# Kernel optimization log

Hardware: AMD Instinct MI355X
Metric: run time of the kernel (lower is better)

The kernel has to match this reference:

```python
import jax, jax.numpy as jnp
import numpy as np

N_NODES = 50000
N_EDGES = 800000
D_IN, D_HID, D_OUT = 128, 128, 64
BN_EPS = 1e-5


def gcn_conv(x, W, b, src, dst, ew, n):
    # PyG GCNConv: out[i] = sum_j norm_ij * (x @ W)[j] + b, with self-loops added
    xw = x @ W                                   # [N, D_out]
    loop = jnp.arange(n)
    s = jnp.concatenate([src, loop])             # add self-loops (weight 1)
    d = jnp.concatenate([dst, loop])
    w = jnp.concatenate([ew, jnp.ones((n,), x.dtype)])
    deg = jax.ops.segment_sum(w, d, num_segments=n)
    dinv = jnp.where(deg > 0, jax.lax.rsqrt(deg), 0.0)
    norm = dinv[s] * w * dinv[d]                 # symmetric normalization
    msg = xw[s] * norm[:, None]                  # gather + scale  [E+N, D_out]
    return jax.ops.segment_sum(msg, d, num_segments=n) + b


def setup_inputs() -> dict:
    key = jax.random.key(0)
    ks = jax.random.split(key, 12)
    x = jax.random.normal(ks[0], (N_NODES, D_IN), dtype=jnp.float32)
    edge_index = jax.random.randint(ks[1], (2, N_EDGES), 0, N_NODES, dtype=jnp.int64)
    edge_weight = jax.random.uniform(ks[2], (N_EDGES,), dtype=jnp.float32)
    W1 = jax.random.normal(ks[3], (D_IN, D_HID), dtype=jnp.float32) * 0.05
    b1 = jnp.zeros((D_HID,), jnp.float32)
    gamma = jnp.ones((D_HID,), jnp.float32)
    beta = jnp.zeros((D_HID,), jnp.float32)
    running_mean = jax.random.normal(ks[4], (D_HID,), dtype=jnp.float32) * 0.1
    running_var = jax.random.uniform(ks[5], (D_HID,), dtype=jnp.float32) + 0.5
    W2 = jax.random.normal(ks[6], (D_HID, D_OUT), dtype=jnp.float32) * 0.05
    b2 = jnp.zeros((D_OUT,), jnp.float32)
    return {"x": x, "edge_index": edge_index, "edge_weight": edge_weight,
            "W1": W1, "b1": b1, "gamma": gamma, "beta": beta,
            "running_mean": running_mean, "running_var": running_var,
            "W2": W2, "b2": b2}


def reference(x, edge_index, edge_weight, W1, b1, gamma, beta,
              running_mean, running_var, W2, b2):
    src, dst = edge_index[0], edge_index[1]
    n = x.shape[0]
    h = gcn_conv(x, W1, b1, src, dst, edge_weight, n)
    # BatchNorm1d in eval mode (running stats); dropout inactive in eval
    h = (h - running_mean) * jax.lax.rsqrt(running_var + BN_EPS) * gamma + beta
    h = jax.nn.relu(h)
    out = gcn_conv(h, W2, b2, src, dst, edge_weight, n)
    return out
```

## Files before the change

### kernel.cpp

```cpp
#include <hip/hip_runtime.h>
#include <hip/hip_fp16.h>

#define BN_EPS 1e-5f
#define PAD 64
#define CAP 4608

typedef __attribute__((ext_vector_type(8))) short short8;
typedef __attribute__((ext_vector_type(4))) float f32x4;

static __device__ __forceinline__ unsigned short f2bf(float f) {
    unsigned u = __float_as_uint(f);
    u += 0x7FFF + ((u >> 16) & 1);
    return (unsigned short)(u >> 16);
}
static __device__ __forceinline__ float bf2f(unsigned short b) {
    return __uint_as_float((unsigned)b << 16);
}
static __device__ __forceinline__ unsigned pk(int s, float w) {
    return ((unsigned)s << 16) | (unsigned)__half_as_ushort(__float2half_rn(w));
}
static __device__ __forceinline__ float pw(unsigned e) {
    return __half2float(__ushort_as_half((unsigned short)(e & 0xFFFFu)));
}

__global__ __launch_bounds__(256) void k_fused(const int* __restrict__ src, const int* __restrict__ dst,
                                               const float* __restrict__ ew,
                                               uint2* __restrict__ bins, int* __restrict__ gcnt,
                                               int e, int gfill, int stride, int nb,
                                               const float* __restrict__ A, const float* __restrict__ W,
                                               unsigned short* __restrict__ C, int n,
                                               const float* __restrict__ b1, const float* __restrict__ gamma,
                                               const float* __restrict__ beta, const float* __restrict__ mean,
                                               const float* __restrict__ var,
                                               float* __restrict__ bnscale, float* __restrict__ bnshift,
                                               const float* __restrict__ W2, unsigned short* __restrict__ w2bf) {
    __shared__ unsigned short W1s[16384];
    int tid = threadIdx.x;
    int b = (int)blockIdx.x;
    int gGemm = (n + 63) / 64;

    bool isFill = ((b % stride) == 0) && (b / stride < gfill);
    if (isFill) {
        int*   lcnt   = (int*)W1s;
        int*   gbase  = lcnt + 256;
        int*   loff   = gbase + 256;
        uint2* sorted = (uint2*)(loff + 256);
        lcnt[tid] = 0;
        __syncthreads();

        int i0 = ((b / stride) * 256 + tid) * 8;
        unsigned pv[8];  int bk[8]; int rk[8]; unsigned dl[8];
        int cnt8 = 0;
        if (i0 + 7 < e) {
            int4   s0 = *(const int4*)(src + i0), s1 = *(const int4*)(src + i0 + 4);
            int4   d0 = *(const int4*)(dst + i0), d1 = *(const int4*)(dst + i0 + 4);
            float4 w0 = *(const float4*)(ew + i0), w1 = *(const float4*)(ew + i0 + 4);
            int   ss[8] = {s0.x, s0.y, s0.z, s0.w, s1.x, s1.y, s1.z, s1.w};
            int   dd[8] = {d0.x, d0.y, d0.z, d0.w, d1.x, d1.y, d1.z, d1.w};
            float ww[8] = {w0.x, w0.y, w0.z, w0.w, w1.x, w1.y, w1.z, w1.w};
            #pragma unroll
            for (int j = 0; j < 8; ++j) {
                int d_ = dd[j];
                bk[j] = d_ >> 8;
                dl[j] = (unsigned)(d_ & 255);
                rk[j] = atomicAdd(&lcnt[bk[j]], 1);
                pv[j] = pk(ss[j], ww[j]);
            }
            cnt8 = 8;
        } else {
            for (int j = 0; j < 8; ++j) {
                int i = i0 + j;
                if (i < e) {
                    int d_ = dst[i];
                    bk[j] = d_ >> 8;
                    dl[j] = (unsigned)(d_ & 255);
                    rk[j] = atomicAdd(&lcnt[bk[j]], 1);
                    pv[j] = pk(src[i], ew[i]);
                    cnt8 = j + 1;
                }
            }
        }
        __syncthreads();
        if (tid < nb) gbase[tid] = atomicAdd(&gcnt[tid], lcnt[tid]);
        int li = lcnt[tid];
        loff[tid] = li;
        __syncthreads();
        #pragma unroll
        for (int off = 1; off < 256; off <<= 1) {
            int v = (tid >= off) ? loff[tid - off] : 0;
            __syncthreads();
            loff[tid] += v;
            __syncthreads();
        }
        int excl = loff[tid] - li;
        __syncthreads();
        loff[tid] = excl;
        __syncthreads();
        for (int j = 0; j < cnt8; ++j) {
            int pos  = gbase[bk[j]] + rk[j];
            int sidx = loff[bk[j]] + rk[j];
            unsigned gp = (pos < CAP) ? ((unsigned)(bk[j] * CAP + pos) | (dl[j] << 24))
                                      : 0xFFFFFFFFu;
            sorted[sidx] = make_uint2(pv[j], gp);
        }
        __syncthreads();
        int total = loff[255] + lcnt[255];
        for (int i = tid; i < total; i += 256) {
            uint2 s = sorted[i];
            if (s.y != 0xFFFFFFFFu)
                bins[s.y & 0x00FFFFFFu] = make_uint2(s.x, s.y >> 24);
        }
        return;
    }

    int fillsBefore = (b == 0) ? 0 : min(gfill, (b - 1) / stride + 1);
    int g = b - fillsBefore;
    if (g == gGemm) {
        if (tid < 128) {
            float sc = gamma[tid] * rsqrtf(var[tid] + BN_EPS);
            bnscale[tid] = sc;
            bnshift[tid] = (b1[tid] - mean[tid]) * sc + beta[tid];
        }
        #pragma unroll
        for (int q = 0; q < 4; ++q) {
            int s = tid * 4 + q;
            int kk = s >> 8, nt = (s >> 6) & 3, lane = s & 63;
            int kb = kk * 32 + ((lane >> 4) << 3);
            int nc = (nt << 4) + (lane & 15);
            ushort4 o0, o1;
            o0.x = f2bf(W2[(kb + 0) * 64 + nc]);
            o0.y = f2bf(W2[(kb + 1) * 64 + nc]);
            o0.z = f2bf(W2[(kb + 2) * 64 + nc]);
            o0.w = f2bf(W2[(kb + 3) * 64 + nc]);
            o1.x = f2bf(W2[(kb + 4) * 64 + nc]);
            o1.y = f2bf(W2[(kb + 5) * 64 + nc]);
            o1.z = f2bf(W2[(kb + 6) * 64 + nc]);
            o1.w = f2bf(W2[(kb + 7) * 64 + nc]);
            ((ushort4*)w2bf)[s * 2]     = o0;
            ((ushort4*)w2bf)[s * 2 + 1] = o1;
        }
        return;
    }

    int row0 = g * 64;

    {
        int k  = tid >> 1;
        int c0 = (tid & 1) * 64;
        int kk = k >> 5, lg = (k >> 3) & 3, ii = k & 7;
        int tbase = kk * 4096 + lg * 128 + ii;
        const float4* Wr = (const float4*)(W + (size_t)k * 128 + c0);
        #pragma unroll
        for (int j = 0; j < 16; ++j) {
            float4 v = Wr[j];
            int n0 = c0 + j * 4;
            W1s[tbase + ((n0 + 0) >> 4) * 512 + ((n0 + 0) & 15) * 8] = f2bf(v.x);
            W1s[tbase + ((n0 + 1) >> 4) * 512 + ((n0 + 1) & 15) * 8] = f2bf(v.y);
            W1s[tbase + ((n0 + 2) >> 4) * 512 + ((n0 + 2) & 15) * 8] = f2bf(v.z);
            W1s[tbase + ((n0 + 3) >> 4) * 512 + ((n0 + 3) & 15) * 8] = f2bf(v.w);
        }
    }
    __syncthreads();

    int w = tid >> 6, lane = tid & 63;
    int arow = row0 + w * 16 + (lane & 15);
    if (arow > n - 1) arow = n - 1;
    const float* xrow = A + (size_t)arow * 128 + ((lane >> 4) * 8);
    const unsigned short* Wl = W1s + (size_t)lane * 8;

    f32x4 z = {0.f, 0.f, 0.f, 0.f};
    f32x4 acc0 = z, acc1 = z, acc2 = z, acc3 = z, acc4 = z, acc5 = z, acc6 = z, acc7 = z;

    #pragma unroll
    for (int kk = 0; kk < 4; ++kk) {
        float4 v0 = *(const float4*)(xrow + kk * 32);
        float4 v1 = *(const float4*)(xrow + kk * 32 + 4);
        short8 a;
        a[0] = (short)f2bf(v0.x); a[1] = (short)f2bf(v0.y);
        a[2] = (short)f2bf(v0.z); a[3] = (short)f2bf(v0.w);
        a[4] = (short)f2bf(v1.x); a[5] = (short)f2bf(v1.y);
        a[6] = (short)f2bf(v1.z); a[7] = (short)f2bf(v1.w);
        const unsigned short* Wk = Wl + kk * 4096;
        short8 b0 = *(const short8*)(Wk);
        short8 b1 = *(const short8*)(Wk + 512);
        short8 b2 = *(const short8*)(Wk + 1024);
        short8 b3 = *(const short8*)(Wk + 1536);
        short8 b4 = *(const short8*)(Wk + 2048);
        short8 b5 = *(const short8*)(Wk + 2560);
        short8 b6 = *(const short8*)(Wk + 3072);
        short8 b7 = *(const short8*)(Wk + 3584);
        acc0 = __builtin_amdgcn_mfma_f32_16x16x32_bf16(a, b0, acc0, 0, 0, 0);
        acc1 = __builtin_amdgcn_mfma_f32_16x16x32_bf16(a, b1, acc1, 0, 0, 0);
        acc2 = __builtin_amdgcn_mfma_f32_16x16x32_bf16(a, b2, acc2, 0, 0, 0);
        acc3 = __builtin_amdgcn_mfma_f32_16x16x32_bf16(a, b3, acc3, 0, 0, 0);
        acc4 = __builtin_amdgcn_mfma_f32_16x16x32_bf16(a, b4, acc4, 0, 0, 0);
        acc5 = __builtin_amdgcn_mfma_f32_16x16x32_bf16(a, b5, acc5, 0, 0, 0);
        acc6 = __builtin_amdgcn_mfma_f32_16x16x32_bf16(a, b6, acc6, 0, 0, 0);
        acc7 = __builtin_amdgcn_mfma_f32_16x16x32_bf16(a, b7, acc7, 0, 0, 0);
    }

    int rw = row0 + w * 16 + ((lane >> 4) << 2);
    int cb = lane & 15;
    #define STORE_NT(av, nt)                                                              \
        if (rw + 0 < n) C[(size_t)(rw + 0) * 128 + (nt)*16 + cb] = f2bf(av[0]);           \
        if (rw + 1 < n) C[(size_t)(rw + 1) * 128 + (nt)*16 + cb] = f2bf(av[1]);           \
        if (rw + 2 < n) C[(size_t)(rw + 2) * 128 + (nt)*16 + cb] = f2bf(av[2]);           \
        if (rw + 3 < n) C[(size_t)(rw + 3) * 128 + (nt)*16 + cb] = f2bf(av[3]);
    STORE_NT(acc0, 0) STORE_NT(acc1, 1) STORE_NT(acc2, 2) STORE_NT(acc3, 3)
    STORE_NT(acc4, 4) STORE_NT(acc5, 5) STORE_NT(acc6, 6) STORE_NT(acc7, 7)
    #undef STORE_NT
}

__global__ __launch_bounds__(256) void k_csr(const uint2* __restrict__ bins, const int* __restrict__ gcnt,
                                             unsigned* __restrict__ pad, int* __restrict__ cnt,
                                             float* __restrict__ dinv, int n) {
    __shared__ unsigned csr[256 * PAD];
    __shared__ int lc[256];
    int tid = threadIdx.x;
    int b = (int)blockIdx.x;
    int node0 = b << 8;
    int nodes = min(256, n - node0);
    lc[tid] = 0;
    __syncthreads();

    int m = gcnt[b];
    if (m > CAP) m = CAP;
    const uint2* seg = bins + (size_t)b * CAP;
    for (int i = tid; i < m; i += 256) {
        uint2 v = seg[i];
        int r = atomicAdd(&lc[v.y], 1);
        if (r < PAD) csr[v.y * PAD + r] = v.x;
    }
    __syncthreads();

    if (tid < nodes) {
        int c = lc[tid];
        cnt[node0 + tid] = c;
        int cc = min(c, PAD);
        float s = 1.0f;
        for (int p = 0; p < cc; ++p) s += pw(csr[tid * PAD + p]);
        dinv[node0 + tid] = rsqrtf(s);
    }
    const uint4* s4 = (const uint4*)csr;
    uint4* d4 = (uint4*)(pad + (size_t)node0 * PAD);
    int tot = nodes * (PAD / 4);
    for (int q = tid; q < tot; q += 256) d4[q] = s4[q];
}

__global__ __launch_bounds__(256) void k_scale(unsigned* __restrict__ pad, const int* __restrict__ cnt,
                                               const float* __restrict__ dinv, int n) {
    int gid = blockIdx.x * 256 + threadIdx.x;
    int node = gid >> 2, q = gid & 3;
    if (node >= n) return;
    int c = min(cnt[node], PAD);
    int p0 = q * 16, p1 = min(p0 + 16, c);
    size_t base = (size_t)node * PAD;
    for (int p = p0; p < p1; ++p) {
        unsigned e = pad[base + p];
        float w = pw(e) * dinv[e >> 16];
        pad[base + p] = (e & 0xFFFF0000u) | (unsigned)__half_as_ushort(__float2half_rn(w));
    }
}

__global__ __launch_bounds__(256) void k_h(const unsigned short* __restrict__ xw, const int* __restrict__ cnt,
                                           const unsigned* __restrict__ pad,
                                           const float* __restrict__ dinv,
                                           const float* __restrict__ scale, const float* __restrict__ shift,
                                           unsigned* __restrict__ h, int n) {
    int grp = threadIdx.x >> 5;
    int lc  = threadIdx.x & 31;
    int node = blockIdx.x * 8 + grp;
    if (node >= n) return;
    const ushort4* X4 = (const ushort4*)xw;
    float di = dinv[node];
    int c = min(cnt[node], PAD);
    size_t base = (size_t)node * PAD;
    ushort4 q0 = X4[(size_t)node * 32 + lc];
    float4 acc0 = make_float4(bf2f(q0.x) * di, bf2f(q0.y) * di, bf2f(q0.z) * di, bf2f(q0.w) * di);
    float4 acc1 = make_float4(0, 0, 0, 0);
    float4 acc2 = make_float4(0, 0, 0, 0);
    float4 acc3 = make_float4(0, 0, 0, 0);
    int p = 0;
    for (; p + 7 < c; p += 8) {
        uint4 ea = *(const uint4*)(pad + base + p);
        uint4 eb = *(const uint4*)(pad + base + p + 4);
        ushort4 r0 = X4[(size_t)(ea.x >> 16) * 32 + lc];
        ushort4 r1 = X4[(size_t)(ea.y >> 16) * 32 + lc];
        ushort4 r2 = X4[(size_t)(ea.z >> 16) * 32 + lc];
        ushort4 r3 = X4[(size_t)(ea.w >> 16) * 32 + lc];
        ushort4 r4 = X4[(size_t)(eb.x >> 16) * 32 + lc];
        ushort4 r5 = X4[(size_t)(eb.y >> 16) * 32 + lc];
        ushort4 r6 = X4[(size_t)(eb.z >> 16) * 32 + lc];
        ushort4 r7 = X4[(size_t)(eb.w >> 16) * 32 + lc];
        float w0 = pw(ea.x), w1 = pw(ea.y), w2 = pw(ea.z), w3 = pw(ea.w);
        float w4 = pw(eb.x), w5 = pw(eb.y), w6 = pw(eb.z), w7 = pw(eb.w);
        acc0.x += w0 * bf2f(r0.x); acc0.y += w0 * bf2f(r0.y); acc0.z += w0 * bf2f(r0.z); acc0.w += w0 * bf2f(r0.w);
        acc1.x += w1 * bf2f(r1.x); acc1.y += w1 * bf2f(r1.y); acc1.z += w1 * bf2f(r1.z); acc1.w += w1 * bf2f(r1.w);
        acc2.x += w2 * bf2f(r2.x); acc2.y += w2 * bf2f(r2.y); acc2.z += w2 * bf2f(r2.z); acc2.w += w2 * bf2f(r2.w);
        acc3.x += w3 * bf2f(r3.x); acc3.y += w3 * bf2f(r3.y); acc3.z += w3 * bf2f(r3.z); acc3.w += w3 * bf2f(r3.w);
        acc0.x += w4 * bf2f(r4.x); acc0.y += w4 * bf2f(r4.y); acc0.z += w4 * bf2f(r4.z); acc0.w += w4 * bf2f(r4.w);
        acc1.x += w5 * bf2f(r5.x); acc1.y += w5 * bf2f(r5.y); acc1.z += w5 * bf2f(r5.z); acc1.w += w5 * bf2f(r5.w);
        acc2.x += w6 * bf2f(r6.x); acc2.y += w6 * bf2f(r6.y); acc2.z += w6 * bf2f(r6.z); acc2.w += w6 * bf2f(r6.w);
        acc3.x += w7 * bf2f(r7.x); acc3.y += w7 * bf2f(r7.y); acc3.z += w7 * bf2f(r7.z); acc3.w += w7 * bf2f(r7.w);
    }
    for (; p + 3 < c; p += 4) {
        uint4 ea = *(const uint4*)(pad + base + p);
        ushort4 r0 = X4[(size_t)(ea.x >> 16) * 32 + lc];
        ushort4 r1 = X4[(size_t)(ea.y >> 16) * 32 + lc];
        ushort4 r2 = X4[(size_t)(ea.z >> 16) * 32 + lc];
        ushort4 r3 = X4[(size_t)(ea.w >> 16) * 32 + lc];
        float w0 = pw(ea.x), w1 = pw(ea.y), w2 = pw(ea.z), w3 = pw(ea.w);
        acc0.x += w0 * bf2f(r0.x); acc0.y += w0 * bf2f(r0.y); acc0.z += w0 * bf2f(r0.z); acc0.w += w0 * bf2f(r0.w);
        acc1.x += w1 * bf2f(r1.x); acc1.y += w1 * bf2f(r1.y); acc1.z += w1 * bf2f(r1.z); acc1.w += w1 * bf2f(r1.w);
        acc2.x += w2 * bf2f(r2.x); acc2.y += w2 * bf2f(r2.y); acc2.z += w2 * bf2f(r2.z); acc2.w += w2 * bf2f(r2.w);
        acc3.x += w3 * bf2f(r3.x); acc3.y += w3 * bf2f(r3.y); acc3.z += w3 * bf2f(r3.z); acc3.w += w3 * bf2f(r3.w);
    }
    for (; p < c; ++p) {
        unsigned e0 = pad[base + p];
        float w0 = pw(e0);
        ushort4 a = X4[(size_t)(e0 >> 16) * 32 + lc];
        acc0.x += w0 * bf2f(a.x); acc0.y += w0 * bf2f(a.y); acc0.z += w0 * bf2f(a.z); acc0.w += w0 * bf2f(a.w);
    }
    acc0.x = (acc0.x + acc1.x + acc2.x + acc3.x) * di;
    acc0.y = (acc0.y + acc1.y + acc2.y + acc3.y) * di;
    acc0.z = (acc0.z + acc1.z + acc2.z + acc3.z) * di;
    acc0.w = (acc0.w + acc1.w + acc2.w + acc3.w) * di;
    float4 Sc = ((const float4*)scale)[lc];
    float4 Sh = ((const float4*)shift)[lc];
    unsigned short r0 = f2bf(fmaxf(acc0.x * Sc.x + Sh.x, 0.0f));
    unsigned short r1 = f2bf(fmaxf(acc0.y * Sc.y + Sh.y, 0.0f));
    unsigned short r2 = f2bf(fmaxf(acc0.z * Sc.z + Sh.z, 0.0f));
    unsigned short r3 = f2bf(fmaxf(acc0.w * Sc.w + Sh.w, 0.0f));
    unsigned hu0 = ((unsigned)r1 << 16) | (unsigned)r0;
    unsigned hu1 = ((unsigned)r3 << 16) | (unsigned)r2;
    *(uint2*)(h + (size_t)node * 64 + lc * 2) = make_uint2(hu0, hu1);
}

__global__ __launch_bounds__(256) void k_gemm2(const unsigned short* __restrict__ h,
                                               const unsigned short* __restrict__ w2bf,
                                               unsigned short* __restrict__ hw2, int n) {
    __shared__ unsigned short W2f[8192];
    int tid = threadIdx.x;
    {
        const uint4* s4 = (const uint4*)w2bf;
        uint4* d4 = (uint4*)W2f;
        #pragma unroll
        for (int q = 0; q < 4; ++q) d4[q * 256 + tid] = s4[q * 256 + tid];
    }
    __syncthreads();

    int w = tid >> 6, lane = tid & 63;
    int row0 = (int)blockIdx.x * 64 + w * 16;
    int ar = row0 + (lane & 15);
    if (ar > n - 1) ar = n - 1;
    const unsigned short* hr = h + (size_t)ar * 128 + ((lane >> 4) * 8);
    const unsigned short* Wl = W2f + (size_t)lane * 8;

    f32x4 z = {0.f, 0.f, 0.f, 0.f};
    f32x4 acc0 = z, acc1 = z, acc2 = z, acc3 = z;
    #pragma unroll
    for (int kk = 0; kk < 4; ++kk) {
        short8 a = *(const short8*)(hr + kk * 32);
        const unsigned short* Wk = Wl + kk * 2048;
        short8 b0 = *(const short8*)(Wk);
        short8 b1 = *(const short8*)(Wk + 512);
        short8 b2 = *(const short8*)(Wk + 1024);
        short8 b3 = *(const short8*)(Wk + 1536);
        acc0 = __builtin_amdgcn_mfma_f32_16x16x32_bf16(a, b0, acc0, 0, 0, 0);
        acc1 = __builtin_amdgcn_mfma_f32_16x16x32_bf16(a, b1, acc1, 0, 0, 0);
        acc2 = __builtin_amdgcn_mfma_f32_16x16x32_bf16(a, b2, acc2, 0, 0, 0);
        acc3 = __builtin_amdgcn_mfma_f32_16x16x32_bf16(a, b3, acc3, 0, 0, 0);
    }
    int rw = row0 + ((lane >> 4) << 2);
    int cb = lane & 15;
    #define ST_NT(av, nt)                                                                 \
        if (rw + 0 < n) hw2[(size_t)(rw + 0) * 64 + (nt)*16 + cb] = f2bf(av[0]);          \
        if (rw + 1 < n) hw2[(size_t)(rw + 1) * 64 + (nt)*16 + cb] = f2bf(av[1]);          \
        if (rw + 2 < n) hw2[(size_t)(rw + 2) * 64 + (nt)*16 + cb] = f2bf(av[2]);          \
        if (rw + 3 < n) hw2[(size_t)(rw + 3) * 64 + (nt)*16 + cb] = f2bf(av[3]);
    ST_NT(acc0, 0) ST_NT(acc1, 1) ST_NT(acc2, 2) ST_NT(acc3, 3)
    #undef ST_NT
}

__global__ __launch_bounds__(256) void k_agg2(const unsigned short* __restrict__ hw, const int* __restrict__ cnt,
                                              const unsigned* __restrict__ pad,
                                              const float* __restrict__ dinv,
                                              const float* __restrict__ b2, float* __restrict__ out, int n) {
    int node = blockIdx.x * 16 + (threadIdx.x >> 4);
    if (node >= n) return;
    int lc = threadIdx.x & 15;
    const ushort4* X4 = (const ushort4*)hw;
    float di = dinv[node];
    int c = min(cnt[node], PAD);
    size_t base = (size_t)node * PAD;
    ushort4 q0 = X4[(size_t)node * 16 + lc];
    float4 acc0 = make_float4(bf2f(q0.x) * di, bf2f(q0.y) * di, bf2f(q0.z) * di, bf2f(q0.w) * di);
    float4 acc1 = make_float4(0, 0, 0, 0);
    float4 acc2 = make_float4(0, 0, 0, 0);
    float4 acc3 = make_float4(0, 0, 0, 0);
    int p = 0;
    for (; p + 7 < c; p += 8) {
        uint4 ea = *(const uint4*)(pad + base + p);
        uint4 eb = *(const uint4*)(pad + base + p + 4);
        ushort4 r0 = X4[(size_t)(ea.x >> 16) * 16 + lc];
        ushort4 r1 = X4[(size_t)(ea.y >> 16) * 16 + lc];
        ushort4 r2 = X4[(size_t)(ea.z >> 16) * 16 + lc];
        ushort4 r3 = X4[(size_t)(ea.w >> 16) * 16 + lc];
        ushort4 r4 = X4[(size_t)(eb.x >> 16) * 16 + lc];
        ushort4 r5 = X4[(size_t)(eb.y >> 16) * 16 + lc];
        ushort4 r6 = X4[(size_t)(eb.z >> 16) * 16 + lc];
        ushort4 r7 = X4[(size_t)(eb.w >> 16) * 16 + lc];
        float w0 = pw(ea.x), w1 = pw(ea.y), w2 = pw(ea.z), w3 = pw(ea.w);
        float w4 = pw(eb.x), w5 = pw(eb.y), w6 = pw(eb.z), w7 = pw(eb.w);
        acc0.x += w0 * bf2f(r0.x); acc0.y += w0 * bf2f(r0.y); acc0.z += w0 * bf2f(r0.z); acc0.w += w0 * bf2f(r0.w);
        acc1.x += w1 * bf2f(r1.x); acc1.y += w1 * bf2f(r1.y); acc1.z += w1 * bf2f(r1.z); acc1.w += w1 * bf2f(r1.w);
        acc2.x += w2 * bf2f(r2.x); acc2.y += w2 * bf2f(r2.y); acc2.z += w2 * bf2f(r2.z); acc2.w += w2 * bf2f(r2.w);
        acc3.x += w3 * bf2f(r3.x); acc3.y += w3 * bf2f(r3.y); acc3.z += w3 * bf2f(r3.z); acc3.w += w3 * bf2f(r3.w);
        acc0.x += w4 * bf2f(r4.x); acc0.y += w4 * bf2f(r4.y); acc0.z += w4 * bf2f(r4.z); acc0.w += w4 * bf2f(r4.w);
        acc1.x += w5 * bf2f(r5.x); acc1.y += w5 * bf2f(r5.y); acc1.z += w5 * bf2f(r5.z); acc1.w += w5 * bf2f(r5.w);
        acc2.x += w6 * bf2f(r6.x); acc2.y += w6 * bf2f(r6.y); acc2.z += w6 * bf2f(r6.z); acc2.w += w6 * bf2f(r6.w);
        acc3.x += w7 * bf2f(r7.x); acc3.y += w7 * bf2f(r7.y); acc3.z += w7 * bf2f(r7.z); acc3.w += w7 * bf2f(r7.w);
    }
    for (; p + 3 < c; p += 4) {
        uint4 ea = *(const uint4*)(pad + base + p);
        ushort4 r0 = X4[(size_t)(ea.x >> 16) * 16 + lc];
        ushort4 r1 = X4[(size_t)(ea.y >> 16) * 16 + lc];
        ushort4 r2 = X4[(size_t)(ea.z >> 16) * 16 + lc];
        ushort4 r3 = X4[(size_t)(ea.w >> 16) * 16 + lc];
        float w0 = pw(ea.x), w1 = pw(ea.y), w2 = pw(ea.z), w3 = pw(ea.w);
        acc0.x += w0 * bf2f(r0.x); acc0.y += w0 * bf2f(r0.y); acc0.z += w0 * bf2f(r0.z); acc0.w += w0 * bf2f(r0.w);
        acc1.x += w1 * bf2f(r1.x); acc1.y += w1 * bf2f(r1.y); acc1.z += w1 * bf2f(r1.z); acc1.w += w1 * bf2f(r1.w);
        acc2.x += w2 * bf2f(r2.x); acc2.y += w2 * bf2f(r2.y); acc2.z += w2 * bf2f(r2.z); acc2.w += w2 * bf2f(r2.w);
        acc3.x += w3 * bf2f(r3.x); acc3.y += w3 * bf2f(r3.y); acc3.z += w3 * bf2f(r3.z); acc3.w += w3 * bf2f(r3.w);
    }
    for (; p < c; ++p) {
        unsigned e0 = pad[base + p];
        float w0 = pw(e0);
        ushort4 a = X4[(size_t)(e0 >> 16) * 16 + lc];
        acc0.x += w0 * bf2f(a.x); acc0.y += w0 * bf2f(a.y); acc0.z += w0 * bf2f(a.z); acc0.w += w0 * bf2f(a.w);
    }
    float4 B = ((const float4*)b2)[lc];
    acc0.x = (acc0.x + acc1.x + acc2.x + acc3.x) * di + B.x;
    acc0.y = (acc0.y + acc1.y + acc2.y + acc3.y) * di + B.y;
    acc0.z = (acc0.z + acc1.z + acc2.z + acc3.z) * di + B.z;
    acc0.w = (acc0.w + acc1.w + acc2.w + acc3.w) * di + B.w;
    ((float4*)out)[(size_t)node * 16 + lc] = acc0;
}


extern "C" void kernel_launch(void* const* d_in, const int* in_sizes, int n_in,
                              void* d_out, int out_size, void* d_ws, size_t ws_size,
                              hipStream_t stream) {
    const float* x     = (const float*)d_in[0];
    const int*   ei    = (const int*)d_in[1];
    const float* ew    = (const float*)d_in[2];
    const float* W1    = (const float*)d_in[3];
    const float* b1    = (const float*)d_in[4];
    const float* gamma = (const float*)d_in[5];
    const float* beta  = (const float*)d_in[6];
    const float* rmean = (const float*)d_in[7];
    const float* rvar  = (const float*)d_in[8];
    const float* W2    = (const float*)d_in[9];
    const float* b2    = (const float*)d_in[10];
    float* out = (float*)d_out;

    int N = in_sizes[0] / 128;
    int E = in_sizes[2];
    const int* src = ei;
    const int* dst = ei + E;
    int NB = (N + 255) >> 8;

    char* p = (char*)d_ws;
    auto carve = [&](size_t bytes) { char* q = p; p += (bytes + 255) & ~(size_t)255; return (void*)q; };
    int*      cnt     = (int*)     carve(sizeof(int) * (size_t)N);
    unsigned* pad     = (unsigned*)carve(sizeof(unsigned) * (size_t)N * PAD);
    float*    dinv    = (float*)   carve(sizeof(float) * (size_t)N);
    float*    bnscale = (float*)   carve(sizeof(float) * 128);
    float*    bnshift = (float*)   carve(sizeof(float) * 128);
    unsigned short* w2bf = (unsigned short*)carve(sizeof(unsigned short) * 128 * 64);
    unsigned short* xw1  = (unsigned short*)carve(sizeof(unsigned short) * (size_t)N * 128);
    unsigned*       hbuf = (unsigned*)      carve(sizeof(unsigned) * (size_t)N * 64);
    unsigned short* hw2  = (unsigned short*)carve(sizeof(unsigned short) * (size_t)N * 64);
    int*      gcnt    = (int*)     carve(sizeof(int) * (size_t)NB);
    uint2*    bins    = (uint2*)   carve(sizeof(uint2) * (size_t)NB * CAP);

    int gFill = (E + 2047) / 2048;
    int gGemm = (N + 63) / 64;
    int T     = gFill + gGemm + 1;
    int S     = T / gFill;
    if (S < 2) S = 2;

    hipMemsetAsync(gcnt, 0, sizeof(int) * (size_t)NB, stream);
    k_fused <<<T, 256, 0, stream>>>(src, dst, ew, bins, gcnt, E, gFill, S, NB,
                                    x, W1, xw1, N,
                                    b1, gamma, beta, rmean, rvar, bnscale, bnshift,
                                    W2, w2bf);
    k_csr   <<<NB, 256, 0, stream>>>(bins, gcnt, pad, cnt, dinv, N);
    k_scale <<<(N * 4 + 255) / 256, 256, 0, stream>>>(pad, cnt, dinv, N);
    k_h     <<<(N + 7) / 8, 256, 0, stream>>>(xw1, cnt, pad, dinv, bnscale, bnshift, hbuf, N);
    k_gemm2 <<<(N + 63) / 64, 256, 0, stream>>>((const unsigned short*)hbuf, w2bf, hw2, N);
    k_agg2  <<<(N + 15) / 16, 256, 0, stream>>>(hw2, cnt, pad, dinv, b2, out, N);
}
```

Measured before the change: 188.8 us.

## Split GEMM1 columns across blocks, halve fill work, widen aggregation gathers

The fused kernel now splits the first GEMM into two 64-column halves per row tile, which halves the shared weight tile and doubles the number of GEMM blocks. Each fill block now bins 4 edges per thread instead of 8, again doubling the block count. Both aggregation kernels now use 16-byte gathers with 8 bf16 features per lane, so each node uses fewer lanes and each block covers more nodes. The 8-wide unrolled edge loop is dropped in favour of a 4-wide loop. The aim is more parallelism and fewer, wider memory transactions, at the cost of more bin atomics and less memory-level parallelism per thread.

```diff
diff --git a/kernel.cpp b/kernel.cpp
--- a/kernel.cpp
+++ b/kernel.cpp
@@ -22,6 +22,15 @@
 static __device__ __forceinline__ float pw(unsigned e) {
     return __half2float(__ushort_as_half((unsigned short)(e & 0xFFFFu)));
 }
+static __device__ __forceinline__ void upk8(uint4 v, float4& a, float4& b) {
+    a.x = bf2f((unsigned short)(v.x & 0xFFFFu)); a.y = bf2f((unsigned short)(v.x >> 16));
+    a.z = bf2f((unsigned short)(v.y & 0xFFFFu)); a.w = bf2f((unsigned short)(v.y >> 16));
+    b.x = bf2f((unsigned short)(v.z & 0xFFFFu)); b.y = bf2f((unsigned short)(v.z >> 16));
+    b.z = bf2f((unsigned short)(v.w & 0xFFFFu)); b.w = bf2f((unsigned short)(v.w >> 16));
+}
+#define FMA8(wv, ra, rb, A, B)                                            \
+    A.x += (wv) * ra.x; A.y += (wv) * ra.y; A.z += (wv) * ra.z; A.w += (wv) * ra.w; \
+    B.x += (wv) * rb.x; B.y += (wv) * rb.y; B.z += (wv) * rb.z; B.w += (wv) * rb.w;
 
 __global__ __launch_bounds__(256) void k_fused(const int* __restrict__ src, const int* __restrict__ dst,
                                                const float* __restrict__ ew,
@@ -34,10 +43,10 @@
                                                const float* __restrict__ var,
                                                float* __restrict__ bnscale, float* __restrict__ bnshift,
                                                const float* __restrict__ W2, unsigned short* __restrict__ w2bf) {
-    __shared__ unsigned short W1s[16384];
+    __shared__ unsigned short W1s[8192];
     int tid = threadIdx.x;
     int b = (int)blockIdx.x;
-    int gGemm = (n + 63) / 64;
+    int gGemm = ((n + 63) / 64) * 2;
 
     bool isFill = ((b % stride) == 0) && (b / stride < gfill);
     if (isFill) {
@@ -48,27 +57,27 @@
         lcnt[tid] = 0;
         __syncthreads();
 
-        int i0 = ((b / stride) * 256 + tid) * 8;
-        unsigned pv[8];  int bk[8]; int rk[8]; unsigned dl[8];
-        int cnt8 = 0;
-        if (i0 + 7 < e) {
-            int4   s0 = *(const int4*)(src + i0), s1 = *(const int4*)(src + i0 + 4);
-            int4   d0 = *(const int4*)(dst + i0), d1 = *(const int4*)(dst + i0 + 4);
-            float4 w0 = *(const float4*)(ew + i0), w1 = *(const float4*)(ew + i0 + 4);
-            int   ss[8] = {s0.x, s0.y, s0.z, s0.w, s1.x, s1.y, s1.z, s1.w};
-            int   dd[8] = {d0.x, d0.y, d0.z, d0.w, d1.x, d1.y, d1.z, d1.w};
-            float ww[8] = {w0.x, w0.y, w0.z, w0.w, w1.x, w1.y, w1.z, w1.w};
+        int i0 = ((b / stride) * 256 + tid) * 4;
+        unsigned pv[4];  int bk[4]; int rk[4]; unsigned dl[4];
+        int cnt4 = 0;
+        if (i0 + 3 < e) {
+            int4   s0 = *(const int4*)(src + i0);
+            int4   d0 = *(const int4*)(dst + i0);
+            float4 w0 = *(const float4*)(ew + i0);
+            int   ss[4] = {s0.x, s0.y, s0.z, s0.w};
+            int   dd[4] = {d0.x, d0.y, d0.z, d0.w};
+            float ww[4] = {w0.x, w0.y, w0.z, w0.w};
             #pragma unroll
-            for (int j = 0; j < 8; ++j) {
+            for (int j = 0; j < 4; ++j) {
                 int d_ = dd[j];
                 bk[j] = d_ >> 8;
                 dl[j] = (unsigned)(d_ & 255);
                 rk[j] = atomicAdd(&lcnt[bk[j]], 1);
                 pv[j] = pk(ss[j], ww[j]);
             }
-            cnt8 = 8;
+            cnt4 = 4;
         } else {
-            for (int j = 0; j < 8; ++j) {
+            for (int j = 0; j < 4; ++j) {
                 int i = i0 + j;
                 if (i < e) {
                     int d_ = dst[i];
@@ -76,7 +85,7 @@
                     dl[j] = (unsigned)(d_ & 255);
                     rk[j] = atomicAdd(&lcnt[bk[j]], 1);
                     pv[j] = pk(src[i], ew[i]);
-                    cnt8 = j + 1;
+                    cnt4 = j + 1;
                 }
             }
         }
@@ -96,7 +105,7 @@
         __syncthreads();
         loff[tid] = excl;
         __syncthreads();
-        for (int j = 0; j < cnt8; ++j) {
+        for (int j = 0; j < cnt4; ++j) {
             int pos  = gbase[bk[j]] + rk[j];
             int sidx = loff[bk[j]] + rk[j];
             unsigned gp = (pos < CAP) ? ((unsigned)(bk[j] * CAP + pos) | (dl[j] << 24))
@@ -142,18 +151,19 @@
         return;
     }
 
-    int row0 = g * 64;
+    int rt = g >> 1, ch = g & 1;
+    int row0 = rt * 64, c0 = ch * 64;
 
     {
         int k  = tid >> 1;
-        int c0 = (tid & 1) * 64;
+        int h0 = (tid & 1) * 32;
         int kk = k >> 5, lg = (k >> 3) & 3, ii = k & 7;
-        int tbase = kk * 4096 + lg * 128 + ii;
-        const float4* Wr = (const float4*)(W + (size_t)k * 128 + c0);
+        int tbase = kk * 2048 + lg * 128 + ii;
+        const float4* Wr = (const float4*)(W + (size_t)k * 128 + c0 + h0);
         #pragma unroll
-        for (int j = 0; j < 16; ++j) {
+        for (int j = 0; j < 8; ++j) {
             float4 v = Wr[j];
-            int n0 = c0 + j * 4;
+            int n0 = h0 + j * 4;
             W1s[tbase + ((n0 + 0) >> 4) * 512 + ((n0 + 0) & 15) * 8] = f2bf(v.x);
             W1s[tbase + ((n0 + 1) >> 4) * 512 + ((n0 + 1) & 15) * 8] = f2bf(v.y);
             W1s[tbase + ((n0 + 2) >> 4) * 512 + ((n0 + 2) & 15) * 8] = f2bf(v.z);
@@ -169,7 +179,7 @@
     const unsigned short* Wl = W1s + (size_t)lane * 8;
 
     f32x4 z = {0.f, 0.f, 0.f, 0.f};
-    f32x4 acc0 = z, acc1 = z, acc2 = z, acc3 = z, acc4 = z, acc5 = z, acc6 = z, acc7 = z;
+    f32x4 acc0 = z, acc1 = z, acc2 = z, acc3 = z;
 
     #pragma unroll
     for (int kk = 0; kk < 4; ++kk) {
@@ -180,34 +190,25 @@
         a[2] = (short)f2bf(v0.z); a[3] = (short)f2bf(v0.w);
         a[4] = (short)f2bf(v1.x); a[5] = (short)f2bf(v1.y);
         a[6] = (short)f2bf(v1.z); a[7] = (short)f2bf(v1.w);
-        const unsigned short* Wk = Wl + kk * 4096;
+        const unsigned short* Wk = Wl + kk * 2048;
         short8 b0 = *(const short8*)(Wk);
         short8 b1 = *(const short8*)(Wk + 512);
         short8 b2 = *(const short8*)(Wk + 1024);
         short8 b3 = *(const short8*)(Wk + 1536);
-        short8 b4 = *(const short8*)(Wk + 2048);
-        short8 b5 = *(const short8*)(Wk + 2560);
-        short8 b6 = *(const short8*)(Wk + 3072);
-        short8 b7 = *(const short8*)(Wk + 3584);
         acc0 = __builtin_amdgcn_mfma_f32_16x16x32_bf16(a, b0, acc0, 0, 0, 0);
         acc1 = __builtin_amdgcn_mfma_f32_16x16x32_bf16(a, b1, acc1, 0, 0, 0);
         acc2 = __builtin_amdgcn_mfma_f32_16x16x32_bf16(a, b2, acc2, 0, 0, 0);
         acc3 = __builtin_amdgcn_mfma_f32_16x16x32_bf16(a, b3, acc3, 0, 0, 0);
-        acc4 = __builtin_amdgcn_mfma_f32_16x16x32_bf16(a, b4, acc4, 0, 0, 0);
-        acc5 = __builtin_amdgcn_mfma_f32_16x16x32_bf16(a, b5, acc5, 0, 0, 0);
-        acc6 = __builtin_amdgcn_mfma_f32_16x16x32_bf16(a, b6, acc6, 0, 0, 0);
-        acc7 = __builtin_amdgcn_mfma_f32_16x16x32_bf16(a, b7, acc7, 0, 0, 0);
     }
 
     int rw = row0 + w * 16 + ((lane >> 4) << 2);
-    int cb = lane & 15;
+    int cb = c0 + (lane & 15);
     #define STORE_NT(av, nt)                                                              \
         if (rw + 0 < n) C[(size_t)(rw + 0) * 128 + (nt)*16 + cb] = f2bf(av[0]);           \
         if (rw + 1 < n) C[(size_t)(rw + 1) * 128 + (nt)*16 + cb] = f2bf(av[1]);           \
         if (rw + 2 < n) C[(size_t)(rw + 2) * 128 + (nt)*16 + cb] = f2bf(av[2]);           \
         if (rw + 3 < n) C[(size_t)(rw + 3) * 128 + (nt)*16 + cb] = f2bf(av[3]);
     STORE_NT(acc0, 0) STORE_NT(acc1, 1) STORE_NT(acc2, 2) STORE_NT(acc3, 3)
-    STORE_NT(acc4, 4) STORE_NT(acc5, 5) STORE_NT(acc6, 6) STORE_NT(acc7, 7)
     #undef STORE_NT
 }
 
@@ -267,73 +268,67 @@
                                            const float* __restrict__ dinv,
                                            const float* __restrict__ scale, const float* __restrict__ shift,
                                            unsigned* __restrict__ h, int n) {
-    int grp = threadIdx.x >> 5;
-    int lc  = threadIdx.x & 31;
-    int node = blockIdx.x * 8 + grp;
+    int grp = threadIdx.x >> 4;
+    int lc  = threadIdx.x & 15;
+    int node = blockIdx.x * 16 + grp;
     if (node >= n) return;
-    const ushort4* X4 = (const ushort4*)xw;
+    const uint4* X = (const uint4*)xw;
     float di = dinv[node];
     int c = min(cnt[node], PAD);
     size_t base = (size_t)node * PAD;
-    ushort4 q0 = X4[(size_t)node * 32 + lc];
-    float4 acc0 = make_float4(bf2f(q0.x) * di, bf2f(q0.y) * di, bf2f(q0.z) * di, bf2f(q0.w) * di);
-    float4 acc1 = make_float4(0, 0, 0, 0);
-    float4 acc2 = make_float4(0, 0, 0, 0);
-    float4 acc3 = make_float4(0, 0, 0, 0);
+    float4 ra, rb;
+    upk8(X[(size_t)node * 16 + lc], ra, rb);
+    float4 A0 = make_float4(ra.x * di, ra.y * di, ra.z * di, ra.w * di);
+    float4 B0 = make_float4(rb.x * di, rb.y * di, rb.z * di, rb.w * di);
+    float4 A1 = make_float4(0, 0, 0, 0), B1 = A1;
+    float4 A2 = A1, B2 = A1, A3 = A1, B3 = A1;
     int p = 0;
-    for (; p + 7 < c; p += 8) {
-        uint4 ea = *(const uint4*)(pad + base + p);
-        uint4 eb = *(const uint4*)(pad + base + p + 4);
-        ushort4 r0 = X4[(size_t)(ea.x >> 16) * 32 + lc];
-        ushort4 r1 = X4[(size_t)(ea.y >> 16) * 32 + lc];
-        ushort4 r2 = X4[(size_t)(ea.z >> 16) * 32 + lc];
-        ushort4 r3 = X4[(size_t)(ea.w >> 16) * 32 + lc];
-        ushort4 r4 = X4[(size_t)(eb.x >> 16) * 32 + lc];
-        ushort4 r5 = X4[(size_t)(eb.y >> 16) * 32 + lc];
-        ushort4 r6 = X4[(size_t)(eb.z >> 16) * 32 + lc];
-        ushort4 r7 = X4[(size_t)(eb.w >> 16) * 32 + lc];
-        float w0 = pw(ea.x), w1 = pw(ea.y), w2 = pw(ea.z), w3 = pw(ea.w);
-        float w4 = pw(eb.x), w5 = pw(eb.y), w6 = pw(eb.z), w7 = pw(eb.w);
-        acc0.x += w0 * bf2f(r0.x); acc0.y += w0 * bf2f(r0.y); acc0.z += w0 * bf2f(r0.z); acc0.w += w0 * bf2f(r0.w);
-        acc1.x += w1 * bf2f(r1.x); acc1.y += w1 * bf2f(r1.y); acc1.z += w1 * bf2f(r1.z); acc1.w += w1 * bf2f(r1.w);
-        acc2.x += w2 * bf2f(r2.x); acc2.y += w2 * bf2f(r2.y); acc2.z += w2 * bf2f(r2.z); acc2.w += w2 * bf2f(r2.w);
-        acc3.x += w3 * bf2f(r3.x); acc3.y += w3 * bf2f(r3.y); acc3.z += w3 * bf2f(r3.z); acc3.w += w3 * bf2f(r3.w);
-        acc0.x += w4 * bf2f(r4.x); acc0.y += w4 * bf2f(r4.y); acc0.z += w4 * bf2f(r4.z); acc0.w += w4 * bf2f(r4.w);
-        acc1.x += w5 * bf2f(r5.x); acc1.y += w5 * bf2f(r5.y); acc1.z += w5 * bf2f(r5.z); acc1.w += w5 * bf2f(r5.w);
-        acc2.x += w6 * bf2f(r6.x); acc2.y += w6 * bf2f(r6.y); acc2.z += w6 * bf2f(r6.z); acc2.w += w6 * bf2f(r6.w);
-        acc3.x += w7 * bf2f(r7.x); acc3.y += w7 * bf2f(r7.y); acc3.z += w7 * bf2f(r7.z); acc3.w += w7 * bf2f(r7.w);
-    }
     for (; p + 3 < c; p += 4) {
-        uint4 ea = *(const uint4*)(pad + base + p);
-        ushort4 r0 = X4[(size_t)(ea.x >> 16) * 32 + lc];
-        ushort4 r1 = X4[(size_t)(ea.y >> 16) * 32 + lc];
-        ushort4 r2 = X4[(size_t)(ea.z >> 16) * 32 + lc];
-        ushort4 r3 = X4[(size_t)(ea.w >> 16) * 32 + lc];
-        float w0 = pw(ea.x), w1 = pw(ea.y), w2 = pw(ea.z), w3 = pw(ea.w);
-        acc0.x += w0 * bf2f(r0.x); acc0.y += w0 * bf2f(r0.y); acc0.z += w0 * bf2f(r0.z); acc0.w += w0 * bf2f(r0.w);
-        acc1.x += w1 * bf2f(r1.x); acc1.y += w1 * bf2f(r1.y); acc1.z += w1 * bf2f(r1.z); acc1.w += w1 * bf2f(r1.w);
-        acc2.x += w2 * bf2f(r2.x); acc2.y += w2 * bf2f(r2.y); acc2.z += w2 * bf2f(r2.z); acc2.w += w2 * bf2f(r2.w);
-        acc3.x += w3 * bf2f(r3.x); acc3.y += w3 * bf2f(r3.y); acc3.z += w3 * bf2f(r3.z); acc3.w += w3 * bf2f(r3.w);
+        uint4 ee = *(const uint4*)(pad + base + p);
+        uint4 r0 = X[(size_t)(ee.x >> 16) * 16 + lc];
+        uint4 r1 = X[(size_t)(ee.y >> 16) * 16 + lc];
+        uint4 r2 = X[(size_t)(ee.z >> 16) * 16 + lc];
+        uint4 r3 = X[(size_t)(ee.w >> 16) * 16 + lc];
+        float w0 = pw(ee.x), w1 = pw(ee.y), w2 = pw(ee.z), w3 = pw(ee.w);
+        float4 a, b;
+        upk8(r0, a, b); FMA8(w0, a, b, A0, B0);
+        upk8(r1, a, b); FMA8(w1, a, b, A1, B1);
+        upk8(r2, a, b); FMA8(w2, a, b, A2, B2);
+        upk8(r3, a, b); FMA8(w3, a, b, A3, B3);
     }
     for (; p < c; ++p) {
         unsigned e0 = pad[base + p];
         float w0 = pw(e0);
-        ushort4 a = X4[(size_t)(e0 >> 16) * 32 + lc];
-        acc0.x += w0 * bf2f(a.x); acc0.y += w0 * bf2f(a.y); acc0.z += w0 * bf2f(a.z); acc0.w += w0 * bf2f(a.w);
-    }
-    acc0.x = (acc0.x + acc1.x + acc2.x + acc3.x) * di;
-    acc0.y = (acc0.y + acc1.y + acc2.y + acc3.y) * di;
-    acc0.z = (acc0.z + acc1.z + acc2.z + acc3.z) * di;
-    acc0.w = (acc0.w + acc1.w + acc2.w + acc3.w) * di;
-    float4 Sc = ((const float4*)scale)[lc];
-    float4 Sh = ((const float4*)shift)[lc];
-    unsigned short r0 = f2bf(fmaxf(acc0.x * Sc.x + Sh.x, 0.0f));
-    unsigned short r1 = f2bf(fmaxf(acc0.y * Sc.y + Sh.y, 0.0f));
-    unsigned short r2 = f2bf(fmaxf(acc0.z * Sc.z + Sh.z, 0.0f));
-    unsigned short r3 = f2bf(fmaxf(acc0.w * Sc.w + Sh.w, 0.0f));
-    unsigned hu0 = ((unsigned)r1 << 16) | (unsigned)r0;
-    unsigned hu1 = ((unsigned)r3 << 16) | (unsigned)r2;
-    *(uint2*)(h + (size_t)node * 64 + lc * 2) = make_uint2(hu0, hu1);
+        float4 a, b;
+        upk8(X[(size_t)(e0 >> 16) * 16 + lc], a, b);
+        FMA8(w0, a, b, A0, B0);
+    }
+    A0.x = (A0.x + A1.x + A2.x + A3.x) * di;
+    A0.y = (A0.y + A1.y + A2.y + A3.y) * di;
+    A0.z = (A0.z + A1.z + A2.z + A3.z) * di;
+    A0.w = (A0.w + A1.w + A2.w + A3.w) * di;
+    B0.x = (B0.x + B1.x + B2.x + B3.x) * di;
+    B0.y = (B0.y + B1.y + B2.y + B3.y) * di;
+    B0.z = (B0.z + B1.z + B2.z + B3.z) * di;
+    B0.w = (B0.w + B1.w + B2.w + B3.w) * di;
+    float4 Sc0 = ((const float4*)scale)[lc * 2];
+    float4 Sc1 = ((const float4*)scale)[lc * 2 + 1];
+    float4 Sh0 = ((const float4*)shift)[lc * 2];
+    float4 Sh1 = ((const float4*)shift)[lc * 2 + 1];
+    unsigned short h0 = f2bf(fmaxf(A0.x * Sc0.x + Sh0.x, 0.0f));
+    unsigned short h1 = f2bf(fmaxf(A0.y * Sc0.y + Sh0.y, 0.0f));
+    unsigned short h2 = f2bf(fmaxf(A0.z * Sc0.z + Sh0.z, 0.0f));
+    unsigned short h3 = f2bf(fmaxf(A0.w * Sc0.w + Sh0.w, 0.0f));
+    unsigned short h4 = f2bf(fmaxf(B0.x * Sc1.x + Sh1.x, 0.0f));
+    unsigned short h5 = f2bf(fmaxf(B0.y * Sc1.y + Sh1.y, 0.0f));
+    unsigned short h6 = f2bf(fmaxf(B0.z * Sc1.z + Sh1.z, 0.0f));
+    unsigned short h7 = f2bf(fmaxf(B0.w * Sc1.w + Sh1.w, 0.0f));
+    uint4 o;
+    o.x = ((unsigned)h1 << 16) | h0;
+    o.y = ((unsigned)h3 << 16) | h2;
+    o.z = ((unsigned)h5 << 16) | h4;
+    o.w = ((unsigned)h7 << 16) | h6;
+    ((uint4*)h)[(size_t)node * 16 + lc] = o;
 }
 
 __global__ __launch_bounds__(256) void k_gemm2(const unsigned short* __restrict__ h,
@@ -386,65 +381,53 @@
                                               const unsigned* __restrict__ pad,
                                               const float* __restrict__ dinv,
                                               const float* __restrict__ b2, float* __restrict__ out, int n) {
-    int node = blockIdx.x * 16 + (threadIdx.x >> 4);
+    int node = blockIdx.x * 32 + (threadIdx.x >> 3);
     if (node >= n) return;
-    int lc = threadIdx.x & 15;
-    const ushort4* X4 = (const ushort4*)hw;
+    int lc = threadIdx.x & 7;
+    const uint4* X = (const uint4*)hw;
     float di = dinv[node];
     int c = min(cnt[node], PAD);
     size_t base = (size_t)node * PAD;
-    ushort4 q0 = X4[(size_t)node * 16 + lc];
-    float4 acc0 = make_float4(bf2f(q0.x) * di, bf2f(q0.y) * di, bf2f(q0.z) * di, bf2f(q0.w) * di);
-    float4 acc1 = make_float4(0, 0, 0, 0);
-    float4 acc2 = make_float4(0, 0, 0, 0);
-    float4 acc3 = make_float4(0, 0, 0, 0);
+    float4 ra, rb;
+    upk8(X[(size_t)node * 8 + lc], ra, rb);
+    float4 A0 = make_float4(ra.x * di, ra.y * di, ra.z * di, ra.w * di);
+    float4 B0 = make_float4(rb.x * di, rb.y * di, rb.z * di, rb.w * di);
+    float4 A1 = make_float4(0, 0, 0, 0), B1 = A1;
+    float4 A2 = A1, B2 = A1, A3 = A1, B3 = A1;
     int p = 0;
-    for (; p + 7 < c; p += 8) {
-        uint4 ea = *(const uint4*)(pad + base + p);
-        uint4 eb = *(const uint4*)(pad + base + p + 4);
-        ushort4 r0 = X4[(size_t)(ea.x >> 16) * 16 + lc];
-        ushort4 r1 = X4[(size_t)(ea.y >> 16) * 16 + lc];
-        ushort4 r2 = X4[(size_t)(ea.z >> 16) * 16 + lc];
-        ushort4 r3 = X4[(size_t)(ea.w >> 16) * 16 + lc];
-        ushort4 r4 = X4[(size_t)(eb.x >> 16) * 16 + lc];
-        ushort4 r5 = X4[(size_t)(eb.y >> 16) * 16 + lc];
-        ushort4 r6 = X4[(size_t)(eb.z >> 16) * 16 + lc];
-        ushort4 r7 = X4[(size_t)(eb.w >> 16) * 16 + lc];
-        float w0 = pw(ea.x), w1 = pw(ea.y), w2 = pw(ea.z), w3 = pw(ea.w);
-        float w4 = pw(eb.x), w5 = pw(eb.y), w6 = pw(eb.z), w7 = pw(eb.w);
-        acc0.x += w0 * bf2f(r0.x); acc0.y += w0 * bf2f(r0.y); acc0.z += w0 * bf2f(r0.z); acc0.w += w0 * bf2f(r0.w);
-        acc1.x += w1 * bf2f(r1.x); acc1.y += w1 * bf2f(r1.y); acc1.z += w1 * bf2f(r1.z); acc1.w += w1 * bf2f(r1.w);
-        acc2.x += w2 * bf2f(r2.x); acc2.y += w2 * bf2f(r2.y); acc2.z += w2 * bf2f(r2.z); acc2.w += w2 * bf2f(r2.w);
-        acc3.x += w3 * bf2f(r3.x); acc3.y += w3 * bf2f(r3.y); acc3.z += w3 * bf2f(r3.z); acc3.w += w3 * bf2f(r3.w);
-        acc0.x += w4 * bf2f(r4.x); acc0.y += w4 * bf2f(r4.y); acc0.z += w4 * bf2f(r4.z); acc0.w += w4 * bf2f(r4.w);
-        acc1.x += w5 * bf2f(r5.x); acc1.y += w5 * bf2f(r5.y); acc1.z += w5 * bf2f(r5.z); acc1.w += w5 * bf2f(r5.w);
-        acc2.x += w6 * bf2f(r6.x); acc2.y += w6 * bf2f(r6.y); acc2.z += w6 * bf2f(r6.z); acc2.w += w6 * bf2f(r6.w);
-        acc3.x += w7 * bf2f(r7.x); acc3.y += w7 * bf2f(r7.y); acc3.z += w7 * bf2f(r7.z); acc3.w += w7 * bf2f(r7.w);
-    }
     for (; p + 3 < c; p += 4) {
-        uint4 ea = *(const uint4*)(pad + base + p);
-        ushort4 r0 = X4[(size_t)(ea.x >> 16) * 16 + lc];
-        ushort4 r1 = X4[(size_t)(ea.y >> 16) * 16 + lc];
-        ushort4 r2 = X4[(size_t)(ea.z >> 16) * 16 + lc];
-        ushort4 r3 = X4[(size_t)(ea.w >> 16) * 16 + lc];
-        float w0 = pw(ea.x), w1 = pw(ea.y), w2 = pw(ea.z), w3 = pw(ea.w);
-        acc0.x += w0 * bf2f(r0.x); acc0.y += w0 * bf2f(r0.y); acc0.z += w0 * bf2f(r0.z); acc0.w += w0 * bf2f(r0.w);
-        acc1.x += w1 * bf2f(r1.x); acc1.y += w1 * bf2f(r1.y); acc1.z += w1 * bf2f(r1.z); acc1.w += w1 * bf2f(r1.w);
-        acc2.x += w2 * bf2f(r2.x); acc2.y += w2 * bf2f(r2.y); acc2.z += w2 * bf2f(r2.z); acc2.w += w2 * bf2f(r2.w);
-        acc3.x += w3 * bf2f(r3.x); acc3.y += w3 * bf2f(r3.y); acc3.z += w3 * bf2f(r3.z); acc3.w += w3 * bf2f(r3.w);
+        uint4 ee = *(const uint4*)(pad + base + p);
+        uint4 r0 = X[(size_t)(ee.x >> 16) * 8 + lc];
+        uint4 r1 = X[(size_t)(ee.y >> 16) * 8 + lc];
+        uint4 r2 = X[(size_t)(ee.z >> 16) * 8 + lc];
+        uint4 r3 = X[(size_t)(ee.w >> 16) * 8 + lc];
+        float w0 = pw(ee.x), w1 = pw(ee.y), w2 = pw(ee.z), w3 = pw(ee.w);
+        float4 a, b;
+        upk8(r0, a, b); FMA8(w0, a, b, A0, B0);
+        upk8(r1, a, b); FMA8(w1, a, b, A1, B1);
+        upk8(r2, a, b); FMA8(w2, a, b, A2, B2);
+        upk8(r3, a, b); FMA8(w3, a, b, A3, B3);
     }
     for (; p < c; ++p) {
         unsigned e0 = pad[base + p];
         float w0 = pw(e0);
-        ushort4 a = X4[(size_t)(e0 >> 16) * 16 + lc];
-        acc0.x += w0 * bf2f(a.x); acc0.y += w0 * bf2f(a.y); acc0.z += w0 * bf2f(a.z); acc0.w += w0 * bf2f(a.w);
-    }
-    float4 B = ((const float4*)b2)[lc];
-    acc0.x = (acc0.x + acc1.x + acc2.x + acc3.x) * di + B.x;
-    acc0.y = (acc0.y + acc1.y + acc2.y + acc3.y) * di + B.y;
-    acc0.z = (acc0.z + acc1.z + acc2.z + acc3.z) * di + B.z;
-    acc0.w = (acc0.w + acc1.w + acc2.w + acc3.w) * di + B.w;
-    ((float4*)out)[(size_t)node * 16 + lc] = acc0;
+        float4 a, b;
+        upk8(X[(size_t)(e0 >> 16) * 8 + lc], a, b);
+        FMA8(w0, a, b, A0, B0);
+    }
+    float4 Ba = ((const float4*)b2)[lc * 2];
+    float4 Bb = ((const float4*)b2)[lc * 2 + 1];
+    float4 o0, o1;
+    o0.x = (A0.x + A1.x + A2.x + A3.x) * di + Ba.x;
+    o0.y = (A0.y + A1.y + A2.y + A3.y) * di + Ba.y;
+    o0.z = (A0.z + A1.z + A2.z + A3.z) * di + Ba.z;
+    o0.w = (A0.w + A1.w + A2.w + A3.w) * di + Ba.w;
+    o1.x = (B0.x + B1.x + B2.x + B3.x) * di + Bb.x;
+    o1.y = (B0.y + B1.y + B2.y + B3.y) * di + Bb.y;
+    o1.z = (B0.z + B1.z + B2.z + B3.z) * di + Bb.z;
+    o1.w = (B0.w + B1.w + B2.w + B3.w) * di + Bb.w;
+    ((float4*)out)[(size_t)node * 16 + lc * 2]     = o0;
+    ((float4*)out)[(size_t)node * 16 + lc * 2 + 1] = o1;
 }
 
 
@@ -484,8 +467,8 @@
     int*      gcnt    = (int*)     carve(sizeof(int) * (size_t)NB);
     uint2*    bins    = (uint2*)   carve(sizeof(uint2) * (size_t)NB * CAP);
 
-    int gFill = (E + 2047) / 2048;
-    int gGemm = (N + 63) / 64;
+    int gFill = (E + 1023) / 1024;
+    int gGemm = ((N + 63) / 64) * 2;
     int T     = gFill + gGemm + 1;
     int S     = T / gFill;
     if (S < 2) S = 2;
@@ -497,7 +480,7 @@
                                     W2, w2bf);
     k_csr   <<<NB, 256, 0, stream>>>(bins, gcnt, pad, cnt, dinv, N);
     k_scale <<<(N * 4 + 255) / 256, 256, 0, stream>>>(pad, cnt, dinv, N);
-    k_h     <<<(N + 7) / 8, 256, 0, stream>>>(xw1, cnt, pad, dinv, bnscale, bnshift, hbuf, N);
+    k_h     <<<(N + 15) / 16, 256, 0, stream>>>(xw1, cnt, pad, dinv, bnscale, bnshift, hbuf, N);
     k_gemm2 <<<(N + 63) / 64, 256, 0, stream>>>((const unsigned short*)hbuf, w2bf, hw2, N);
-    k_agg2  <<<(N + 15) / 16, 256, 0, stream>>>(hw2, cnt, pad, dinv, b2, out, N);
-}
+    k_agg2  <<<(N + 31) / 32, 256, 0, stream>>>(hw2, cnt, pad, dinv, b2, out, N);
+}
```

After: 189.3 us. Within noise of the previous version (+0.3%).
